# Performance work log

Measured on AMD Instinct MI355X. Metric: run time of the kernel, lower is better.

## Reference

```python
import jax, jax.numpy as jnp
import numpy as np

B, EMB, HID, IN_DIM, STEP = 4096, 256, 256, 128, 128


def setup_inputs() -> dict:
    key = jax.random.key(0)
    ks = jax.random.split(key, 9)
    s1 = 1.0 / np.sqrt(HID)   # torch LSTMCell init: U(-1/sqrt(hidden), 1/sqrt(hidden))
    s2 = 1.0 / np.sqrt(IN_DIM)
    u = lambda k, shape, s: jax.random.uniform(k, shape, jnp.float32, -s, s)
    return {
        "emb_inp": jax.random.normal(ks[0], (B, EMB), jnp.float32),
        # cell1: LSTMCell(EMB -> HID), gate order i,f,g,o
        "W_ih1": u(ks[1], (4 * HID, EMB), s1),
        "W_hh1": u(ks[2], (4 * HID, HID), s1),
        "b_ih1": u(ks[3], (4 * HID,), s1),
        "b_hh1": u(ks[4], (4 * HID,), s1),
        # cell2: LSTMCell(HID -> IN_DIM)
        "W_ih2": u(ks[5], (4 * IN_DIM, HID), s2),
        "W_hh2": u(ks[6], (4 * IN_DIM, IN_DIM), s2),
        "b_ih2": u(ks[7], (4 * IN_DIM,), s2),
        "b_hh2": u(ks[8], (4 * IN_DIM,), s2),
    }


def _lstm_gates(gates, c):
    # torch.nn.LSTMCell gate order: input, forget, cell(g), output
    i, f, g, o = jnp.split(gates, 4, axis=-1)
    c_new = jax.nn.sigmoid(f) * c + jax.nn.sigmoid(i) * jnp.tanh(g)
    h_new = jax.nn.sigmoid(o) * jnp.tanh(c_new)
    return h_new, c_new


def reference(emb_inp, W_ih1, W_hh1, b_ih1, b_hh1, W_ih2, W_hh2, b_ih2, b_hh2):
    batch = emb_inp.shape[0]
    hid = W_hh1.shape[1]
    in_dim = W_hh2.shape[1]
    dt = emb_inp.dtype
    # the same emb_inp is fed at every step -> precompute input-gate preactivations once
    x1 = emb_inp @ W_ih1.T + b_ih1 + b_hh1              # [B, 4*HID]
    b2 = b_ih2 + b_hh2

    init = (jnp.zeros((batch, hid), dt), jnp.zeros((batch, hid), dt),
            jnp.zeros((batch, in_dim), dt), jnp.zeros((batch, in_dim), dt))

    def step_fn(carry, _):
        h0, c0, h1, c1 = carry
        h0, c0 = _lstm_gates(x1 + h0 @ W_hh1.T, c0)
        h1, c1 = _lstm_gates(h0 @ W_ih2.T + b2 + h1 @ W_hh2.T, c1)
        return (h0, c0, h1, c1), h1

    _, ys = jax.lax.scan(step_fn, init, None, length=STEP)  # [STEP, B, IN_DIM]
    return jnp.transpose(ys, (1, 0, 2))                     # [B, STEP, IN_DIM]
```

## Files before the change

### kernel.cpp

```cpp
#include <hip/hip_runtime.h>

typedef __attribute__((ext_vector_type(8))) short bf16x8;
typedef __attribute__((ext_vector_type(4))) short bf16x4;
typedef __attribute__((ext_vector_type(4))) float f32x4;

__device__ __forceinline__ short f2bf(float f) {
  union { float f; unsigned u; } v; v.f = f;
  unsigned r = v.u + 0x7fffu + ((v.u >> 16) & 1u);
  return (short)(r >> 16);
}
__device__ __forceinline__ float sigm(float x) {
  float e = exp2f(-1.44269504f * x);
  return __builtin_amdgcn_rcpf(1.0f + e);
}
__device__ __forceinline__ float tanh_f(float x) {
  float e = exp2f(-2.88539008f * x);
  return __builtin_fmaf(2.0f, __builtin_amdgcn_rcpf(1.0f + e), -1.0f);
}
__device__ __forceinline__ f32x4 splat4(float b){ f32x4 v = {b,b,b,b}; return v; }

__device__ __forceinline__ void ld_b128_sc0(bf16x8* d, const void* p) {
  asm volatile("global_load_dwordx4 %0, %1, off sc0" : "=&v"(*d) : "v"(p));
}
__device__ __forceinline__ void vm_drain_sched() {
  asm volatile("s_waitcnt vmcnt(0)" ::: "memory");
  __builtin_amdgcn_sched_barrier(0);
}

#define R1S   0
#define R2AS  262144
#define R2BS  393216
#define R1IS  458752
#define CTRL_B 1441792
#define H0X_B  1462272
#define H1X_B  5656576

#define H0S 57344
#define H1S 65536
#define OUTS 69632

__global__ __launch_bounds__(256) void pack_w(
    const float* __restrict__ W_ih1, const float* __restrict__ W_hh1,
    const float* __restrict__ W_ih2, const float* __restrict__ W_hh2,
    short* __restrict__ wp) {
  int s = blockIdx.x * 256 + threadIdx.x;
  if (blockIdx.x == 0) {
    unsigned* c = (unsigned*)((char*)wp + CTRL_B);
    #pragma unroll
    for (int k = 0; k < 20; ++k) c[threadIdx.x + k * 256] = 0u;
  }
  if (s >= 90112) return;
  const float* src; int row, K, k0, l;
  if (s < 32768) {
    int mm = s >> 11, r = s & 2047, nf = r >> 9, kc = (r >> 6) & 7; l = r & 63;
    int a = nf >> 1, gh = nf & 1, ul = (l & 15) >> 1, gp = l & 1;
    row = (gh*2+gp)*256 + mm*16 + a*8 + ul; K = 256; k0 = kc*32 + (l>>4)*8; src = W_hh1;
  } else if (s < 49152) {
    int s2 = s - 32768, mm = s2 >> 10, r = s2 & 1023, gh = r >> 9, kc = (r >> 6) & 7; l = r & 63;
    int ul = (l & 15) >> 1, gp = l & 1;
    row = (gh*2+gp)*128 + mm*8 + ul; K = 256; k0 = kc*32 + (l>>4)*8; src = W_ih2;
  } else if (s < 57344) {
    int s3 = s - 49152, mm = s3 >> 9, r = s3 & 511, gh = r >> 8, kc = (r >> 6) & 3; l = r & 63;
    int ul = (l & 15) >> 1, gp = l & 1;
    row = (gh*2+gp)*128 + mm*8 + ul; K = 128; k0 = kc*32 + (l>>4)*8; src = W_hh2;
  } else {
    int s4 = s - 57344, mm = s4 >> 11, r = s4 & 2047, nf = r >> 9, kc = (r >> 6) & 7; l = r & 63;
    int a = nf >> 1, gh = nf & 1, ul = (l & 15) >> 1, gp = l & 1;
    row = (gh*2+gp)*256 + mm*16 + a*8 + ul; K = 256; k0 = kc*32 + (l>>4)*8; src = W_ih1;
  }
  const float* p = src + (size_t)row * K + k0;
  bf16x8 o;
  #pragma unroll
  for (int e = 0; e < 8; ++e) o[e] = f2bf(p[e]);
  *(bf16x8*)(wp + (size_t)s * 8) = o;
}

__global__ __launch_bounds__(512, 2) void lstm_persist(
    const float* __restrict__ emb, const float* __restrict__ b_ih1,
    const float* __restrict__ b_hh1, const float* __restrict__ b_ih2,
    const float* __restrict__ b_hh2, char* __restrict__ ws,
    float* __restrict__ out) {
  extern __shared__ __align__(16) short ldsW[];
  char* ldsB = (char*)ldsW;
  const short* wp = (const short*)ws;
  unsigned* ctrl = (unsigned*)(ws + CTRL_B);
  __shared__ unsigned s_gm;
  const int tid = threadIdx.x, w = tid >> 6, l = tid & 63, l15 = l & 15, l4 = l >> 4;
  const int ul = l15 >> 1, gp = l15 & 1;

  if (tid == 0) {
    unsigned xcc;
    asm volatile("s_getreg_b32 %0, hwreg(HW_REG_XCC_ID)" : "=s"(xcc));
    xcc &= 7u;
    unsigned slot = atomicAdd(&ctrl[xcc * 32], 1u);
    s_gm = ((xcc * 2u + ((slot >> 4) & 1u)) << 8) | (slot & 15u);
  }
  __syncthreads();
  const int group = s_gm >> 8, member = s_gm & 255;

  {
    const char* wpB = (const char*)wp;
    #pragma unroll
    for (int it = 0; it < 7; ++it) {
      int byte = (tid + it * 512) * 16;
      const char* src;
      if (byte < 32768)      src = wpB + (size_t)R1S * 2  + member * 32768 + byte;
      else if (byte < 49152) src = wpB + (size_t)R2AS * 2 + member * 16384 + (byte - 32768);
      else                   src = wpB + (size_t)R2BS * 2 + member * 8192  + (byte - 49152);
      *(f32x4*)(ldsB + byte) = *(const f32x4*)src;
    }
  }
  float b2[2];
  #pragma unroll
  for (int gh = 0; gh < 2; ++gh) {
    int rw = (gh*2+gp)*128 + member*8 + ul;
    b2[gh] = b_ih2[rw] + b_hh2[rw];
  }
  float b1[4];
  #pragma unroll
  for (int nf = 0; nf < 4; ++nf) {
    int rw = ((nf&1)*2+gp)*256 + member*16 + (nf>>1)*8 + ul;
    b1[nf] = b_ih1[rw] + b_hh1[rw];
  }
  __syncthreads();

  const int grow0 = group * 256;
  const int rw0 = w * 32;
  f32x4 x1[2][4];
  #pragma unroll
  for (int m = 0; m < 2; ++m)
    #pragma unroll
    for (int nf = 0; nf < 4; ++nf) x1[m][nf] = splat4(b1[nf]);
  #pragma unroll
  for (int kc = 0; kc < 8; ++kc) {
    bf16x8 af[2];
    #pragma unroll
    for (int m = 0; m < 2; ++m) {
      const float* ep = emb + (size_t)(grow0 + rw0 + m*16 + l15) * 256 + kc*32 + l4*8;
      f32x4 lo = *(const f32x4*)ep, hi = *(const f32x4*)(ep + 4);
      bf16x8 t8;
      #pragma unroll
      for (int e = 0; e < 4; ++e) { t8[e] = f2bf(lo[e]); t8[e+4] = f2bf(hi[e]); }
      af[m] = t8;
    }
    #pragma unroll
    for (int nf = 0; nf < 4; ++nf) {
      bf16x8 bb = *(const bf16x8*)(wp + R1IS + (((size_t)member*4 + nf)*8 + kc)*512 + l*8);
      x1[0][nf] = __builtin_amdgcn_mfma_f32_16x16x32_bf16(af[0], bb, x1[0][nf], 0, 0, 0);
      x1[1][nf] = __builtin_amdgcn_mfma_f32_16x16x32_bf16(af[1], bb, x1[1][nf], 0, 0, 0);
    }
  }

  bf16x8 a0[2][8], a1[2][4];
  const bf16x8 ZB = {0,0,0,0,0,0,0,0};
  #pragma unroll
  for (int m = 0; m < 2; ++m) {
    #pragma unroll
    for (int kc = 0; kc < 8; ++kc) a0[m][kc] = ZB;
    #pragma unroll
    for (int kc = 0; kc < 4; ++kc) a1[m][kc] = ZB;
  }
  float c0[2][2][2] = {};
  float c1[2][2] = {};

  unsigned* flgA = &ctrl[512 + group * 64];
  unsigned* flgB = flgA + 32;
  char* h0x = ws + H0X_B;
  char* h1x = ws + H1X_B;

  #pragma unroll 1
  for (int u = 0; u <= 128; ++u) {
    if (u < 128) {
      vm_drain_sched();
      f32x4 acc1[2][4];
      #pragma unroll
      for (int m = 0; m < 2; ++m)
        #pragma unroll
        for (int nf = 0; nf < 4; ++nf) acc1[m][nf] = x1[m][nf];
      #pragma unroll
      for (int nf = 0; nf < 4; ++nf)
        #pragma unroll
        for (int kc = 0; kc < 8; ++kc) {
          bf16x8 bb = *(const bf16x8*)(ldsW + (nf*8 + kc)*512 + l*8);
          acc1[0][nf] = __builtin_amdgcn_mfma_f32_16x16x32_bf16(a0[0][kc], bb, acc1[0][nf], 0,0,0);
          acc1[1][nf] = __builtin_amdgcn_mfma_f32_16x16x32_bf16(a0[1][kc], bb, acc1[1][nf], 0,0,0);
        }
      #pragma unroll
      for (int m = 0; m < 2; ++m)
        #pragma unroll
        for (int a = 0; a < 2; ++a) {
          f32x4 v0 = acc1[m][a*2+0], v1 = acc1[m][a*2+1];
          #pragma unroll
          for (int rr = 0; rr < 2; ++rr) {
            float s0 = gp ? v0[rr] : v0[2+rr];
            float s1 = gp ? v1[rr] : v1[2+rr];
            float p0 = __shfl_xor(s0, 1, 64);
            float p1 = __shfl_xor(s1, 1, 64);
            float o0 = gp ? v0[2+rr] : v0[rr];
            float o1 = gp ? v1[2+rr] : v1[rr];
            float iv = gp ? p0 : o0, fv = gp ? o0 : p0;
            float gv = gp ? p1 : o1, ov = gp ? o1 : p1;
            float c = sigm(fv) * c0[m][a][rr] + sigm(iv) * tanh_f(gv);
            c0[m][a][rr] = c;
            float h = sigm(ov) * tanh_f(c);
            int row = rw0 + m*16 + l4*4 + gp*2 + rr;
            *(short*)(ldsB + H0S + row*32 + (a*8 + ul)*2) = f2bf(h);
          }
        }
      {
        char* h0w = h0x + ((size_t)(u & 1) * 16 + group) * 131072;
        int prow = rw0 + (l >> 1);
        int off = prow*32 + (l & 1)*16;
        bf16x8 v = *(const bf16x8*)(ldsB + H0S + off);
        *(bf16x8*)(h0w + member*8192 + off) = v;
      }
      asm volatile("s_waitcnt vmcnt(0)" ::: "memory");
      __syncthreads();
      if (tid == 0)
        __hip_atomic_store(&flgA[member], (unsigned)(u + 1),
                           __ATOMIC_RELAXED, __HIP_MEMORY_SCOPE_AGENT);
    }
    f32x4 acc2[2][2];
    if (u >= 1) {
      if (u >= 2) {
        unsigned tgt = (unsigned)(u - 1); int z = 0;
        while (true) {
          unsigned v = __hip_atomic_load(&flgB[l15], __ATOMIC_RELAXED, __HIP_MEMORY_SCOPE_AGENT);
          if (__all((int)(v >= tgt))) break;
          __builtin_amdgcn_s_sleep(1);
          if (++z > (1 << 20)) break;
        }
        __builtin_amdgcn_sched_barrier(0);
        const char* h1r = h1x + ((size_t)((u - 2) & 1) * 16 + group) * 65536;
        #pragma unroll
        for (int m = 0; m < 2; ++m)
          #pragma unroll
          for (int kc = 0; kc < 4; ++kc)
            ld_b128_sc0(&a1[m][kc], h1r + (kc*4 + l4)*4096 + (rw0 + m*16 + l15)*16);
        vm_drain_sched();
      }
      #pragma unroll
      for (int m = 0; m < 2; ++m)
        #pragma unroll
        for (int gh = 0; gh < 2; ++gh) acc2[m][gh] = splat4(b2[gh]);
      #pragma unroll
      for (int gh = 0; gh < 2; ++gh)
        #pragma unroll
        for (int kc = 0; kc < 8; ++kc) {
          bf16x8 bb = *(const bf16x8*)(ldsW + 16384 + (gh*8 + kc)*512 + l*8);
          acc2[0][gh] = __builtin_amdgcn_mfma_f32_16x16x32_bf16(a0[0][kc], bb, acc2[0][gh], 0,0,0);
          acc2[1][gh] = __builtin_amdgcn_mfma_f32_16x16x32_bf16(a0[1][kc], bb, acc2[1][gh], 0,0,0);
        }
      #pragma unroll
      for (int gh = 0; gh < 2; ++gh)
        #pragma unroll
        for (int kc = 0; kc < 4; ++kc) {
          bf16x8 bb = *(const bf16x8*)(ldsW + 24576 + (gh*4 + kc)*512 + l*8);
          acc2[0][gh] = __builtin_amdgcn_mfma_f32_16x16x32_bf16(a1[0][kc], bb, acc2[0][gh], 0,0,0);
          acc2[1][gh] = __builtin_amdgcn_mfma_f32_16x16x32_bf16(a1[1][kc], bb, acc2[1][gh], 0,0,0);
        }
    }
    if (u < 128) {
      unsigned tgt = (unsigned)(u + 1); int z = 0;
      while (true) {
        unsigned v = __hip_atomic_load(&flgA[l15], __ATOMIC_RELAXED, __HIP_MEMORY_SCOPE_AGENT);
        if (__all((int)(v >= tgt))) break;
        __builtin_amdgcn_s_sleep(1);
        if (++z > (1 << 20)) break;
      }
      __builtin_amdgcn_sched_barrier(0);
      const char* h0r = h0x + ((size_t)(u & 1) * 16 + group) * 131072;
      #pragma unroll
      for (int m = 0; m < 2; ++m)
        #pragma unroll
        for (int kc = 0; kc < 8; ++kc)
          ld_b128_sc0(&a0[m][kc],
                      h0r + (kc*2 + (l4 >> 1))*8192 + (rw0 + m*16 + l15)*32 + (l4 & 1)*16);
      __builtin_amdgcn_sched_barrier(0);
    }
    if (u >= 1) {
      const int t = u - 1;
      #pragma unroll
      for (int m = 0; m < 2; ++m) {
        f32x4 v0 = acc2[m][0], v1 = acc2[m][1];
        #pragma unroll
        for (int rr = 0; rr < 2; ++rr) {
          float s0 = gp ? v0[rr] : v0[2+rr];
          float s1 = gp ? v1[rr] : v1[2+rr];
          float p0 = __shfl_xor(s0, 1, 64);
          float p1 = __shfl_xor(s1, 1, 64);
          float o0 = gp ? v0[2+rr] : v0[rr];
          float o1 = gp ? v1[2+rr] : v1[rr];
          float iv = gp ? p0 : o0, fv = gp ? o0 : p0;
          float gv = gp ? p1 : o1, ov = gp ? o1 : p1;
          float c = sigm(fv) * c1[m][rr] + sigm(iv) * tanh_f(gv);
          c1[m][rr] = c;
          float h = sigm(ov) * tanh_f(c);
          int row = rw0 + m*16 + l4*4 + gp*2 + rr;
          *(short*)(ldsB + H1S + row*16 + ul*2) = f2bf(h);
          *(float*)(ldsB + OUTS + row*32 + ul*4) = h;
        }
      }
      if (u < 128) {
        char* h1w = h1x + ((size_t)(t & 1) * 16 + group) * 65536;
        int prow = rw0 + (l >> 1);
        int off = prow*16 + (l & 1)*8;
        bf16x4 v = *(const bf16x4*)(ldsB + H1S + off);
        *(bf16x4*)(h1w + member*4096 + off) = v;
        asm volatile("s_waitcnt vmcnt(0)" ::: "memory");
        __syncthreads();
        if (tid == 0)
          __hip_atomic_store(&flgB[member], (unsigned)u,
                             __ATOMIC_RELAXED, __HIP_MEMORY_SCOPE_AGENT);
      }
      {
        int prow = rw0 + (l >> 1);
        f32x4 v = *(const f32x4*)(ldsB + OUTS + prow*32 + (l & 1)*16);
        float* op = out + (size_t)(grow0 + prow) * 16384 + t*128 + member*8 + (l & 1)*4;
        __builtin_nontemporal_store(v, (f32x4*)op);
      }
    }
  }
}

extern "C" void kernel_launch(void* const* d_in, const int* in_sizes, int n_in,
                              void* d_out, int out_size, void* d_ws, size_t ws_size,
                              hipStream_t stream) {
  const float* emb   = (const float*)d_in[0];
  const float* W_ih1 = (const float*)d_in[1];
  const float* W_hh1 = (const float*)d_in[2];
  const float* b_ih1 = (const float*)d_in[3];
  const float* b_hh1 = (const float*)d_in[4];
  const float* W_ih2 = (const float*)d_in[5];
  const float* W_hh2 = (const float*)d_in[6];
  const float* b_ih2 = (const float*)d_in[7];
  const float* b_hh2 = (const float*)d_in[8];
  char* ws = (char*)d_ws;
  float* out = (float*)d_out;

  hipFuncSetAttribute((const void*)lstm_persist,
                      hipFuncAttributeMaxDynamicSharedMemorySize, 98304);
  pack_w<<<352, 256, 0, stream>>>(W_ih1, W_hh1, W_ih2, W_hh2, (short*)d_ws);
  lstm_persist<<<256, 512, 98304, stream>>>(emb, b_ih1, b_hh1, b_ih2, b_hh2, ws, out);
}
```

Baseline: 1.022 ms.

## Split each block's rows into two halves with separate flags to pipeline steps

Each block's 256 batch rows are split into two 128-row halves, each with its own flag set, so the layer-1 compute, publish and sync for one half can overlap with waiting on the other half and with layer-2 work. Layer 2 likewise runs per half, waiting on per-half flags and loading h1 per half. The aim is to shorten the critical-path latency of the cross-block handoff in this persistent recurrent kernel. The cost is twice as many __syncthreads and flag stores per step, and narrower global stores (bf16x4, u32 and f32x2 instead of wider vectors).

```diff
diff --git a/kernel.cpp b/kernel.cpp
--- a/kernel.cpp
+++ b/kernel.cpp
@@ -3,6 +3,7 @@
 typedef __attribute__((ext_vector_type(8))) short bf16x8;
 typedef __attribute__((ext_vector_type(4))) short bf16x4;
 typedef __attribute__((ext_vector_type(4))) float f32x4;
+typedef __attribute__((ext_vector_type(2))) float f32x2;
 
 __device__ __forceinline__ short f2bf(float f) {
   union { float f; unsigned u; } v; v.f = f;
@@ -87,6 +88,7 @@
   __shared__ unsigned s_gm;
   const int tid = threadIdx.x, w = tid >> 6, l = tid & 63, l15 = l & 15, l4 = l >> 4;
   const int ul = l15 >> 1, gp = l15 & 1;
+  const int rw16 = w * 16;
 
   if (tid == 0) {
     unsigned xcc;
@@ -125,46 +127,36 @@
   __syncthreads();
 
   const int grow0 = group * 256;
-  const int rw0 = w * 32;
   f32x4 x1[2][4];
   #pragma unroll
-  for (int m = 0; m < 2; ++m)
-    #pragma unroll
-    for (int nf = 0; nf < 4; ++nf) x1[m][nf] = splat4(b1[nf]);
-  #pragma unroll
-  for (int kc = 0; kc < 8; ++kc) {
-    bf16x8 af[2];
-    #pragma unroll
-    for (int m = 0; m < 2; ++m) {
-      const float* ep = emb + (size_t)(grow0 + rw0 + m*16 + l15) * 256 + kc*32 + l4*8;
+  for (int k = 0; k < 2; ++k)
+    #pragma unroll
+    for (int nf = 0; nf < 4; ++nf) x1[k][nf] = splat4(b1[nf]);
+  #pragma unroll
+  for (int k = 0; k < 2; ++k)
+    #pragma unroll
+    for (int kc = 0; kc < 8; ++kc) {
+      const float* ep = emb + (size_t)(grow0 + k*128 + rw16 + l15) * 256 + kc*32 + l4*8;
       f32x4 lo = *(const f32x4*)ep, hi = *(const f32x4*)(ep + 4);
-      bf16x8 t8;
+      bf16x8 af;
       #pragma unroll
-      for (int e = 0; e < 4; ++e) { t8[e] = f2bf(lo[e]); t8[e+4] = f2bf(hi[e]); }
-      af[m] = t8;
+      for (int e = 0; e < 4; ++e) { af[e] = f2bf(lo[e]); af[e+4] = f2bf(hi[e]); }
+      #pragma unroll
+      for (int nf = 0; nf < 4; ++nf) {
+        bf16x8 bb = *(const bf16x8*)(wp + R1IS + (((size_t)member*4 + nf)*8 + kc)*512 + l*8);
+        x1[k][nf] = __builtin_amdgcn_mfma_f32_16x16x32_bf16(af, bb, x1[k][nf], 0, 0, 0);
+      }
     }
-    #pragma unroll
-    for (int nf = 0; nf < 4; ++nf) {
-      bf16x8 bb = *(const bf16x8*)(wp + R1IS + (((size_t)member*4 + nf)*8 + kc)*512 + l*8);
-      x1[0][nf] = __builtin_amdgcn_mfma_f32_16x16x32_bf16(af[0], bb, x1[0][nf], 0, 0, 0);
-      x1[1][nf] = __builtin_amdgcn_mfma_f32_16x16x32_bf16(af[1], bb, x1[1][nf], 0, 0, 0);
-    }
-  }
-
-  bf16x8 a0[2][8], a1[2][4];
+
+  bf16x8 a0[2][8];
   const bf16x8 ZB = {0,0,0,0,0,0,0,0};
   #pragma unroll
-  for (int m = 0; m < 2; ++m) {
-    #pragma unroll
-    for (int kc = 0; kc < 8; ++kc) a0[m][kc] = ZB;
-    #pragma unroll
-    for (int kc = 0; kc < 4; ++kc) a1[m][kc] = ZB;
-  }
+  for (int k = 0; k < 2; ++k)
+    #pragma unroll
+    for (int kc = 0; kc < 8; ++kc) a0[k][kc] = ZB;
   float c0[2][2][2] = {};
   float c1[2][2] = {};
 
-  unsigned* flgA = &ctrl[512 + group * 64];
-  unsigned* flgB = flgA + 32;
   char* h0x = ws + H0X_B;
   char* h1x = ws + H1X_B;
 
@@ -172,24 +164,22 @@
   for (int u = 0; u <= 128; ++u) {
     if (u < 128) {
       vm_drain_sched();
-      f32x4 acc1[2][4];
       #pragma unroll
-      for (int m = 0; m < 2; ++m)
-        #pragma unroll
-        for (int nf = 0; nf < 4; ++nf) acc1[m][nf] = x1[m][nf];
-      #pragma unroll
-      for (int nf = 0; nf < 4; ++nf)
-        #pragma unroll
-        for (int kc = 0; kc < 8; ++kc) {
-          bf16x8 bb = *(const bf16x8*)(ldsW + (nf*8 + kc)*512 + l*8);
-          acc1[0][nf] = __builtin_amdgcn_mfma_f32_16x16x32_bf16(a0[0][kc], bb, acc1[0][nf], 0,0,0);
-          acc1[1][nf] = __builtin_amdgcn_mfma_f32_16x16x32_bf16(a0[1][kc], bb, acc1[1][nf], 0,0,0);
-        }
-      #pragma unroll
-      for (int m = 0; m < 2; ++m)
+      for (int k = 0; k < 2; ++k) {
+        unsigned* flgA = &ctrl[512 + group*128 + k*32];
+        f32x4 acc1[4];
+        #pragma unroll
+        for (int nf = 0; nf < 4; ++nf) acc1[nf] = x1[k][nf];
+        #pragma unroll
+        for (int nf = 0; nf < 4; ++nf)
+          #pragma unroll
+          for (int kc = 0; kc < 8; ++kc) {
+            bf16x8 bb = *(const bf16x8*)(ldsW + (nf*8 + kc)*512 + l*8);
+            acc1[nf] = __builtin_amdgcn_mfma_f32_16x16x32_bf16(a0[k][kc], bb, acc1[nf], 0,0,0);
+          }
         #pragma unroll
         for (int a = 0; a < 2; ++a) {
-          f32x4 v0 = acc1[m][a*2+0], v1 = acc1[m][a*2+1];
+          f32x4 v0 = acc1[a*2+0], v1 = acc1[a*2+1];
           #pragma unroll
           for (int rr = 0; rr < 2; ++rr) {
             float s0 = gp ? v0[rr] : v0[2+rr];
@@ -200,89 +190,88 @@
             float o1 = gp ? v1[2+rr] : v1[rr];
             float iv = gp ? p0 : o0, fv = gp ? o0 : p0;
             float gv = gp ? p1 : o1, ov = gp ? o1 : p1;
-            float c = sigm(fv) * c0[m][a][rr] + sigm(iv) * tanh_f(gv);
-            c0[m][a][rr] = c;
+            float c = sigm(fv) * c0[k][a][rr] + sigm(iv) * tanh_f(gv);
+            c0[k][a][rr] = c;
             float h = sigm(ov) * tanh_f(c);
-            int row = rw0 + m*16 + l4*4 + gp*2 + rr;
+            int row = k*128 + rw16 + l4*4 + gp*2 + rr;
             *(short*)(ldsB + H0S + row*32 + (a*8 + ul)*2) = f2bf(h);
           }
         }
-      {
-        char* h0w = h0x + ((size_t)(u & 1) * 16 + group) * 131072;
-        int prow = rw0 + (l >> 1);
-        int off = prow*32 + (l & 1)*16;
-        bf16x8 v = *(const bf16x8*)(ldsB + H0S + off);
-        *(bf16x8*)(h0w + member*8192 + off) = v;
-      }
-      asm volatile("s_waitcnt vmcnt(0)" ::: "memory");
-      __syncthreads();
-      if (tid == 0)
-        __hip_atomic_store(&flgA[member], (unsigned)(u + 1),
-                           __ATOMIC_RELAXED, __HIP_MEMORY_SCOPE_AGENT);
+        {
+          char* h0w = h0x + ((size_t)(u & 1) * 16 + group) * 131072;
+          int prow = k*128 + rw16 + (l >> 2);
+          int off = prow*32 + (l & 3)*8;
+          bf16x4 v = *(const bf16x4*)(ldsB + H0S + off);
+          *(bf16x4*)(h0w + member*8192 + off) = v;
+        }
+        asm volatile("s_waitcnt vmcnt(0)" ::: "memory");
+        __syncthreads();
+        if (tid == 0)
+          __hip_atomic_store(&flgA[member], (unsigned)(u + 1),
+                             __ATOMIC_RELAXED, __HIP_MEMORY_SCOPE_AGENT);
+      }
     }
-    f32x4 acc2[2][2];
-    if (u >= 1) {
-      if (u >= 2) {
-        unsigned tgt = (unsigned)(u - 1); int z = 0;
+    #pragma unroll
+    for (int k = 0; k < 2; ++k) {
+      unsigned* flgA = &ctrl[512 + group*128 + k*32];
+      unsigned* flgB = &ctrl[512 + group*128 + 64 + k*32];
+      f32x4 acc2[2];
+      if (u >= 1) {
+        bf16x8 a1k[4];
+        if (u >= 2) {
+          unsigned tgt = (unsigned)(u - 1); int z = 0;
+          while (true) {
+            unsigned v = __hip_atomic_load(&flgB[l15], __ATOMIC_RELAXED, __HIP_MEMORY_SCOPE_AGENT);
+            if (__all((int)(v >= tgt))) break;
+            __builtin_amdgcn_s_sleep(1);
+            if (++z > (1 << 20)) break;
+          }
+          __builtin_amdgcn_sched_barrier(0);
+          const char* h1r = h1x + ((size_t)((u - 2) & 1) * 16 + group) * 65536;
+          #pragma unroll
+          for (int kc = 0; kc < 4; ++kc)
+            ld_b128_sc0(&a1k[kc], h1r + (kc*4 + l4)*4096 + (k*128 + rw16 + l15)*16);
+          vm_drain_sched();
+        } else {
+          #pragma unroll
+          for (int kc = 0; kc < 4; ++kc) a1k[kc] = ZB;
+        }
+        #pragma unroll
+        for (int gh = 0; gh < 2; ++gh) acc2[gh] = splat4(b2[gh]);
+        #pragma unroll
+        for (int gh = 0; gh < 2; ++gh)
+          #pragma unroll
+          for (int kc = 0; kc < 8; ++kc) {
+            bf16x8 bb = *(const bf16x8*)(ldsW + 16384 + (gh*8 + kc)*512 + l*8);
+            acc2[gh] = __builtin_amdgcn_mfma_f32_16x16x32_bf16(a0[k][kc], bb, acc2[gh], 0,0,0);
+          }
+        #pragma unroll
+        for (int gh = 0; gh < 2; ++gh)
+          #pragma unroll
+          for (int kc = 0; kc < 4; ++kc) {
+            bf16x8 bb = *(const bf16x8*)(ldsW + 24576 + (gh*4 + kc)*512 + l*8);
+            acc2[gh] = __builtin_amdgcn_mfma_f32_16x16x32_bf16(a1k[kc], bb, acc2[gh], 0,0,0);
+          }
+      }
+      if (u < 128) {
+        unsigned tgt = (unsigned)(u + 1); int z = 0;
         while (true) {
-          unsigned v = __hip_atomic_load(&flgB[l15], __ATOMIC_RELAXED, __HIP_MEMORY_SCOPE_AGENT);
+          unsigned v = __hip_atomic_load(&flgA[l15], __ATOMIC_RELAXED, __HIP_MEMORY_SCOPE_AGENT);
           if (__all((int)(v >= tgt))) break;
           __builtin_amdgcn_s_sleep(1);
           if (++z > (1 << 20)) break;
         }
         __builtin_amdgcn_sched_barrier(0);
-        const char* h1r = h1x + ((size_t)((u - 2) & 1) * 16 + group) * 65536;
-        #pragma unroll
-        for (int m = 0; m < 2; ++m)
-          #pragma unroll
-          for (int kc = 0; kc < 4; ++kc)
-            ld_b128_sc0(&a1[m][kc], h1r + (kc*4 + l4)*4096 + (rw0 + m*16 + l15)*16);
-        vm_drain_sched();
-      }
-      #pragma unroll
-      for (int m = 0; m < 2; ++m)
-        #pragma unroll
-        for (int gh = 0; gh < 2; ++gh) acc2[m][gh] = splat4(b2[gh]);
-      #pragma unroll
-      for (int gh = 0; gh < 2; ++gh)
-        #pragma unroll
-        for (int kc = 0; kc < 8; ++kc) {
-          bf16x8 bb = *(const bf16x8*)(ldsW + 16384 + (gh*8 + kc)*512 + l*8);
-          acc2[0][gh] = __builtin_amdgcn_mfma_f32_16x16x32_bf16(a0[0][kc], bb, acc2[0][gh], 0,0,0);
-          acc2[1][gh] = __builtin_amdgcn_mfma_f32_16x16x32_bf16(a0[1][kc], bb, acc2[1][gh], 0,0,0);
-        }
-      #pragma unroll
-      for (int gh = 0; gh < 2; ++gh)
-        #pragma unroll
-        for (int kc = 0; kc < 4; ++kc) {
-          bf16x8 bb = *(const bf16x8*)(ldsW + 24576 + (gh*4 + kc)*512 + l*8);
-          acc2[0][gh] = __builtin_amdgcn_mfma_f32_16x16x32_bf16(a1[0][kc], bb, acc2[0][gh], 0,0,0);
-          acc2[1][gh] = __builtin_amdgcn_mfma_f32_16x16x32_bf16(a1[1][kc], bb, acc2[1][gh], 0,0,0);
-        }
-    }
-    if (u < 128) {
-      unsigned tgt = (unsigned)(u + 1); int z = 0;
-      while (true) {
-        unsigned v = __hip_atomic_load(&flgA[l15], __ATOMIC_RELAXED, __HIP_MEMORY_SCOPE_AGENT);
-        if (__all((int)(v >= tgt))) break;
-        __builtin_amdgcn_s_sleep(1);
-        if (++z > (1 << 20)) break;
-      }
-      __builtin_amdgcn_sched_barrier(0);
-      const char* h0r = h0x + ((size_t)(u & 1) * 16 + group) * 131072;
-      #pragma unroll
-      for (int m = 0; m < 2; ++m)
+        const char* h0r = h0x + ((size_t)(u & 1) * 16 + group) * 131072;
         #pragma unroll
         for (int kc = 0; kc < 8; ++kc)
-          ld_b128_sc0(&a0[m][kc],
-                      h0r + (kc*2 + (l4 >> 1))*8192 + (rw0 + m*16 + l15)*32 + (l4 & 1)*16);
-      __builtin_amdgcn_sched_barrier(0);
-    }
-    if (u >= 1) {
-      const int t = u - 1;
-      #pragma unroll
-      for (int m = 0; m < 2; ++m) {
-        f32x4 v0 = acc2[m][0], v1 = acc2[m][1];
+          ld_b128_sc0(&a0[k][kc],
+                      h0r + (kc*2 + (l4 >> 1))*8192 + (k*128 + rw16 + l15)*32 + (l4 & 1)*16);
+        __builtin_amdgcn_sched_barrier(0);
+      }
+      if (u >= 1) {
+        const int t = u - 1;
+        f32x4 v0 = acc2[0], v1 = acc2[1];
         #pragma unroll
         for (int rr = 0; rr < 2; ++rr) {
           float s0 = gp ? v0[rr] : v0[2+rr];
@@ -293,31 +282,30 @@
           float o1 = gp ? v1[2+rr] : v1[rr];
           float iv = gp ? p0 : o0, fv = gp ? o0 : p0;
           float gv = gp ? p1 : o1, ov = gp ? o1 : p1;
-          float c = sigm(fv) * c1[m][rr] + sigm(iv) * tanh_f(gv);
-          c1[m][rr] = c;
+          float c = sigm(fv) * c1[k][rr] + sigm(iv) * tanh_f(gv);
+          c1[k][rr] = c;
           float h = sigm(ov) * tanh_f(c);
-          int row = rw0 + m*16 + l4*4 + gp*2 + rr;
+          int row = k*128 + rw16 + l4*4 + gp*2 + rr;
           *(short*)(ldsB + H1S + row*16 + ul*2) = f2bf(h);
           *(float*)(ldsB + OUTS + row*32 + ul*4) = h;
         }
-      }
-      if (u < 128) {
-        char* h1w = h1x + ((size_t)(t & 1) * 16 + group) * 65536;
-        int prow = rw0 + (l >> 1);
-        int off = prow*16 + (l & 1)*8;
-        bf16x4 v = *(const bf16x4*)(ldsB + H1S + off);
-        *(bf16x4*)(h1w + member*4096 + off) = v;
-        asm volatile("s_waitcnt vmcnt(0)" ::: "memory");
-        __syncthreads();
-        if (tid == 0)
-          __hip_atomic_store(&flgB[member], (unsigned)u,
-                             __ATOMIC_RELAXED, __HIP_MEMORY_SCOPE_AGENT);
-      }
-      {
-        int prow = rw0 + (l >> 1);
-        f32x4 v = *(const f32x4*)(ldsB + OUTS + prow*32 + (l & 1)*16);
-        float* op = out + (size_t)(grow0 + prow) * 16384 + t*128 + member*8 + (l & 1)*4;
-        __builtin_nontemporal_store(v, (f32x4*)op);
+        int prow = k*128 + rw16 + (l >> 2);
+        if (u < 128) {
+          char* h1w = h1x + ((size_t)(t & 1) * 16 + group) * 65536;
+          int off = prow*16 + (l & 3)*4;
+          unsigned v = *(const unsigned*)(ldsB + H1S + off);
+          *(unsigned*)(h1w + member*4096 + off) = v;
+          asm volatile("s_waitcnt vmcnt(0)" ::: "memory");
+          __syncthreads();
+          if (tid == 0)
+            __hip_atomic_store(&flgB[member], (unsigned)u,
+                               __ATOMIC_RELAXED, __HIP_MEMORY_SCOPE_AGENT);
+        }
+        {
+          f32x2 v = *(const f32x2*)(ldsB + OUTS + prow*32 + (l & 3)*8);
+          float* op = out + (size_t)(grow0 + prow) * 16384 + t*128 + member*8 + (l & 3)*2;
+          __builtin_nontemporal_store(v, (f32x2*)op);
+        }
       }
     }
   }
```

Result: slower. 1.146 ms (+12.1%).

## Pack cell1 weights gate-major and keep cell2 weights in registers

Applied to the files above, without the earlier changes.

Repacks W_hh1 and W_ih1 so each MFMA output tile holds a single gate for 16 consecutive hidden units. Each lane then has i,f,g,o for the same element directly, which removes the lane-pair shuffles and selects from the cell1 gate epilogue. Cell2 weight fragments (W_ih2, W_hh2) now stay in VGPRs for the whole kernel instead of being reread from LDS every step, so LDS shrinks to only the W_hh1 tile. The cost is 24 extra bf16x8 registers per lane, which may pressure occupancy under launch_bounds(512,2) or cause spills.

```diff
diff --git a/kernel.cpp b/kernel.cpp
--- a/kernel.cpp
+++ b/kernel.cpp
@@ -35,9 +35,9 @@
 #define H0X_B  1462272
 #define H1X_B  5656576
 
-#define H0S 57344
-#define H1S 65536
-#define OUTS 69632
+#define H0S 32768
+#define H1S 40960
+#define OUTS 45056
 
 __global__ __launch_bounds__(256) void pack_w(
     const float* __restrict__ W_ih1, const float* __restrict__ W_hh1,
@@ -52,9 +52,8 @@
   if (s >= 90112) return;
   const float* src; int row, K, k0, l;
   if (s < 32768) {
-    int mm = s >> 11, r = s & 2047, nf = r >> 9, kc = (r >> 6) & 7; l = r & 63;
-    int a = nf >> 1, gh = nf & 1, ul = (l & 15) >> 1, gp = l & 1;
-    row = (gh*2+gp)*256 + mm*16 + a*8 + ul; K = 256; k0 = kc*32 + (l>>4)*8; src = W_hh1;
+    int mm = s >> 11, r = s & 2047, g = r >> 9, kc = (r >> 6) & 7; l = r & 63;
+    row = g*256 + mm*16 + (l & 15); K = 256; k0 = kc*32 + (l>>4)*8; src = W_hh1;
   } else if (s < 49152) {
     int s2 = s - 32768, mm = s2 >> 10, r = s2 & 1023, gh = r >> 9, kc = (r >> 6) & 7; l = r & 63;
     int ul = (l & 15) >> 1, gp = l & 1;
@@ -64,9 +63,8 @@
     int ul = (l & 15) >> 1, gp = l & 1;
     row = (gh*2+gp)*128 + mm*8 + ul; K = 128; k0 = kc*32 + (l>>4)*8; src = W_hh2;
   } else {
-    int s4 = s - 57344, mm = s4 >> 11, r = s4 & 2047, nf = r >> 9, kc = (r >> 6) & 7; l = r & 63;
-    int a = nf >> 1, gh = nf & 1, ul = (l & 15) >> 1, gp = l & 1;
-    row = (gh*2+gp)*256 + mm*16 + a*8 + ul; K = 256; k0 = kc*32 + (l>>4)*8; src = W_ih1;
+    int s4 = s - 57344, mm = s4 >> 11, r = s4 & 2047, g = r >> 9, kc = (r >> 6) & 7; l = r & 63;
+    row = g*256 + mm*16 + (l & 15); K = 256; k0 = kc*32 + (l>>4)*8; src = W_ih1;
   }
   const float* p = src + (size_t)row * K + k0;
   bf16x8 o;
@@ -101,14 +99,20 @@
   {
     const char* wpB = (const char*)wp;
     #pragma unroll
-    for (int it = 0; it < 7; ++it) {
+    for (int it = 0; it < 4; ++it) {
       int byte = (tid + it * 512) * 16;
-      const char* src;
-      if (byte < 32768)      src = wpB + (size_t)R1S * 2  + member * 32768 + byte;
-      else if (byte < 49152) src = wpB + (size_t)R2AS * 2 + member * 16384 + (byte - 32768);
-      else                   src = wpB + (size_t)R2BS * 2 + member * 8192  + (byte - 49152);
-      *(f32x4*)(ldsB + byte) = *(const f32x4*)src;
-    }
+      *(f32x4*)(ldsB + byte) = *(const f32x4*)(wpB + member * 32768 + byte);
+    }
+  }
+  bf16x8 wr2a[2][8], wr2b[2][4];
+  #pragma unroll
+  for (int gh = 0; gh < 2; ++gh) {
+    #pragma unroll
+    for (int kc = 0; kc < 8; ++kc)
+      wr2a[gh][kc] = *(const bf16x8*)(wp + R2AS + (((size_t)member*2 + gh)*8 + kc)*512 + l*8);
+    #pragma unroll
+    for (int kc = 0; kc < 4; ++kc)
+      wr2b[gh][kc] = *(const bf16x8*)(wp + R2BS + (((size_t)member*2 + gh)*4 + kc)*512 + l*8);
   }
   float b2[2];
   #pragma unroll
@@ -118,9 +122,9 @@
   }
   float b1[4];
   #pragma unroll
-  for (int nf = 0; nf < 4; ++nf) {
-    int rw = ((nf&1)*2+gp)*256 + member*16 + (nf>>1)*8 + ul;
-    b1[nf] = b_ih1[rw] + b_hh1[rw];
+  for (int g = 0; g < 4; ++g) {
+    int rw = g*256 + member*16 + l15;
+    b1[g] = b_ih1[rw] + b_hh1[rw];
   }
   __syncthreads();
 
@@ -130,7 +134,7 @@
   #pragma unroll
   for (int m = 0; m < 2; ++m)
     #pragma unroll
-    for (int nf = 0; nf < 4; ++nf) x1[m][nf] = splat4(b1[nf]);
+    for (int g = 0; g < 4; ++g) x1[m][g] = splat4(b1[g]);
   #pragma unroll
   for (int kc = 0; kc < 8; ++kc) {
     bf16x8 af[2];
@@ -144,10 +148,10 @@
       af[m] = t8;
     }
     #pragma unroll
-    for (int nf = 0; nf < 4; ++nf) {
-      bf16x8 bb = *(const bf16x8*)(wp + R1IS + (((size_t)member*4 + nf)*8 + kc)*512 + l*8);
-      x1[0][nf] = __builtin_amdgcn_mfma_f32_16x16x32_bf16(af[0], bb, x1[0][nf], 0, 0, 0);
-      x1[1][nf] = __builtin_amdgcn_mfma_f32_16x16x32_bf16(af[1], bb, x1[1][nf], 0, 0, 0);
+    for (int g = 0; g < 4; ++g) {
+      bf16x8 bb = *(const bf16x8*)(wp + R1IS + (((size_t)member*4 + g)*8 + kc)*512 + l*8);
+      x1[0][g] = __builtin_amdgcn_mfma_f32_16x16x32_bf16(af[0], bb, x1[0][g], 0, 0, 0);
+      x1[1][g] = __builtin_amdgcn_mfma_f32_16x16x32_bf16(af[1], bb, x1[1][g], 0, 0, 0);
     }
   }
 
@@ -160,7 +164,7 @@
     #pragma unroll
     for (int kc = 0; kc < 4; ++kc) a1[m][kc] = ZB;
   }
-  float c0[2][2][2] = {};
+  float c0[2][4] = {};
   float c1[2][2] = {};
 
   unsigned* flgA = &ctrl[512 + group * 64];
@@ -176,36 +180,26 @@
       #pragma unroll
       for (int m = 0; m < 2; ++m)
         #pragma unroll
-        for (int nf = 0; nf < 4; ++nf) acc1[m][nf] = x1[m][nf];
-      #pragma unroll
-      for (int nf = 0; nf < 4; ++nf)
+        for (int g = 0; g < 4; ++g) acc1[m][g] = x1[m][g];
+      #pragma unroll
+      for (int g = 0; g < 4; ++g)
         #pragma unroll
         for (int kc = 0; kc < 8; ++kc) {
-          bf16x8 bb = *(const bf16x8*)(ldsW + (nf*8 + kc)*512 + l*8);
-          acc1[0][nf] = __builtin_amdgcn_mfma_f32_16x16x32_bf16(a0[0][kc], bb, acc1[0][nf], 0,0,0);
-          acc1[1][nf] = __builtin_amdgcn_mfma_f32_16x16x32_bf16(a0[1][kc], bb, acc1[1][nf], 0,0,0);
+          bf16x8 bb = *(const bf16x8*)(ldsW + (g*8 + kc)*512 + l*8);
+          acc1[0][g] = __builtin_amdgcn_mfma_f32_16x16x32_bf16(a0[0][kc], bb, acc1[0][g], 0,0,0);
+          acc1[1][g] = __builtin_amdgcn_mfma_f32_16x16x32_bf16(a0[1][kc], bb, acc1[1][g], 0,0,0);
         }
       #pragma unroll
       for (int m = 0; m < 2; ++m)
         #pragma unroll
-        for (int a = 0; a < 2; ++a) {
-          f32x4 v0 = acc1[m][a*2+0], v1 = acc1[m][a*2+1];
-          #pragma unroll
-          for (int rr = 0; rr < 2; ++rr) {
-            float s0 = gp ? v0[rr] : v0[2+rr];
-            float s1 = gp ? v1[rr] : v1[2+rr];
-            float p0 = __shfl_xor(s0, 1, 64);
-            float p1 = __shfl_xor(s1, 1, 64);
-            float o0 = gp ? v0[2+rr] : v0[rr];
-            float o1 = gp ? v1[2+rr] : v1[rr];
-            float iv = gp ? p0 : o0, fv = gp ? o0 : p0;
-            float gv = gp ? p1 : o1, ov = gp ? o1 : p1;
-            float c = sigm(fv) * c0[m][a][rr] + sigm(iv) * tanh_f(gv);
-            c0[m][a][rr] = c;
-            float h = sigm(ov) * tanh_f(c);
-            int row = rw0 + m*16 + l4*4 + gp*2 + rr;
-            *(short*)(ldsB + H0S + row*32 + (a*8 + ul)*2) = f2bf(h);
-          }
+        for (int r = 0; r < 4; ++r) {
+          float iv = acc1[m][0][r], fv = acc1[m][1][r];
+          float gv = acc1[m][2][r], ov = acc1[m][3][r];
+          float c = sigm(fv) * c0[m][r] + sigm(iv) * tanh_f(gv);
+          c0[m][r] = c;
+          float h = sigm(ov) * tanh_f(c);
+          int row = rw0 + m*16 + l4*4 + r;
+          *(short*)(ldsB + H0S + row*32 + l15*2) = f2bf(h);
         }
       {
         char* h0w = h0x + ((size_t)(u & 1) * 16 + group) * 131072;
@@ -247,17 +241,15 @@
       for (int gh = 0; gh < 2; ++gh)
         #pragma unroll
         for (int kc = 0; kc < 8; ++kc) {
-          bf16x8 bb = *(const bf16x8*)(ldsW + 16384 + (gh*8 + kc)*512 + l*8);
-          acc2[0][gh] = __builtin_amdgcn_mfma_f32_16x16x32_bf16(a0[0][kc], bb, acc2[0][gh], 0,0,0);
-          acc2[1][gh] = __builtin_amdgcn_mfma_f32_16x16x32_bf16(a0[1][kc], bb, acc2[1][gh], 0,0,0);
+          acc2[0][gh] = __builtin_amdgcn_mfma_f32_16x16x32_bf16(a0[0][kc], wr2a[gh][kc], acc2[0][gh], 0,0,0);
+          acc2[1][gh] = __builtin_amdgcn_mfma_f32_16x16x32_bf16(a0[1][kc], wr2a[gh][kc], acc2[1][gh], 0,0,0);
         }
       #pragma unroll
       for (int gh = 0; gh < 2; ++gh)
         #pragma unroll
         for (int kc = 0; kc < 4; ++kc) {
-          bf16x8 bb = *(const bf16x8*)(ldsW + 24576 + (gh*4 + kc)*512 + l*8);
-          acc2[0][gh] = __builtin_amdgcn_mfma_f32_16x16x32_bf16(a1[0][kc], bb, acc2[0][gh], 0,0,0);
-          acc2[1][gh] = __builtin_amdgcn_mfma_f32_16x16x32_bf16(a1[1][kc], bb, acc2[1][gh], 0,0,0);
+          acc2[0][gh] = __builtin_amdgcn_mfma_f32_16x16x32_bf16(a1[0][kc], wr2b[gh][kc], acc2[0][gh], 0,0,0);
+          acc2[1][gh] = __builtin_amdgcn_mfma_f32_16x16x32_bf16(a1[1][kc], wr2b[gh][kc], acc2[1][gh], 0,0,0);
         }
     }
     if (u < 128) {
```

Result: slower. 1.760 ms (+72.2%).
